# Performance work log

Measured on AMD Instinct MI355X. Metric: run time of the kernel, lower is better.

The kernel has to match this reference:

```python
import jax, jax.numpy as jnp
import numpy as np

N = 100000          # num nodes
K = 50              # num sampled neighbors per node (num_samples)
F_IN = 128          # in_features
F_OUT = 128         # out_features


def setup_inputs() -> dict:
    key = jax.random.key(0)
    k1, k2, k3, k4 = jax.random.split(key, 4)
    x = jax.random.normal(k1, (N, F_IN), dtype=jnp.float32)
    neighbors = jax.random.randint(k2, (N, K), 0, N, dtype=jnp.int64)
    stdv = 1.0 / np.sqrt(F_OUT)
    weight = jax.random.uniform(k3, (2 * F_IN, F_OUT), dtype=jnp.float32,
                                minval=-stdv, maxval=stdv)
    bias = jax.random.uniform(k4, (F_OUT,), dtype=jnp.float32,
                              minval=-stdv, maxval=stdv)
    return {"x": x, "neighbors": neighbors, "weight": weight, "bias": bias}


def reference(x, neighbors, weight, bias):
    # aggregate: gather sampled neighbor features and mean-reduce (aggregator='mean')
    # x[neighbors]: [N, K, F_IN] -> mean over K -> [N, F_IN]
    agg = jnp.mean(jnp.take(x, neighbors, axis=0), axis=1)
    # concat self + aggregated, linear, bias, relu
    h = jnp.concatenate([x, agg], axis=1)  # [N, 2*F_IN]
    out = h @ weight + bias                # [N, F_OUT]
    return jax.nn.relu(out)
```

## Files before the change

### kernel.cpp

```cpp
#include <hip/hip_runtime.h>
#include <hip/hip_bf16.h>
#include <stdint.h>

#define NN 100000
#define KN 50
#define FIN 128
#define FOUT 128
#define BM 64

typedef __attribute__((ext_vector_type(8))) short bf16x8;
typedef __attribute__((ext_vector_type(4))) float f32x4;
typedef __attribute__((ext_vector_type(2))) float f32x2;

__device__ __forceinline__ uint16_t f2b(float f){
  uint32_t x = __builtin_bit_cast(uint32_t, f);
  x += 0x7fffu + ((x >> 16) & 1u);
  return (uint16_t)(x >> 16);
}

__global__ void cast_fp8_kernel(const float* __restrict__ x, uint32_t* __restrict__ xf8){
  int i = blockIdx.x * blockDim.x + threadIdx.x;
  float4 v = *(const float4*)(x + (size_t)i * 4);
  uint32_t p = 0;
  p = __builtin_amdgcn_cvt_pk_fp8_f32(v.x, v.y, p, false);
  p = __builtin_amdgcn_cvt_pk_fp8_f32(v.z, v.w, p, true);
  xf8[i] = p;
}

__global__ void pack_w_kernel(const float* __restrict__ w, uint16_t* __restrict__ wp){
  int kt = blockIdx.x >> 3, nt = blockIdx.x & 7;
  int lane = threadIdx.x;
  int col = nt * 16 + (lane & 15);
  int k0  = kt * 32 + ((lane >> 4) << 3);
  uint16_t vals[8];
  #pragma unroll
  for (int i = 0; i < 8; i++) vals[i] = f2b(w[(k0 + i) * FOUT + col]);
  *(uint4*)(wp + ((size_t)(kt * 8 + nt) * 64 + lane) * 8) = *(const uint4*)vals;
}

__global__ void detect_kernel(const int* __restrict__ nb, int* __restrict__ flag){
  int i = blockIdx.x * blockDim.x + threadIdx.x;
  if (nb[2 * i + 1] != 0) *flag = 1;
}

#define CVT8(ACC, v)                                           \
  ACC[0] += __builtin_amdgcn_cvt_pk_f32_fp8((v).x, false);     \
  ACC[1] += __builtin_amdgcn_cvt_pk_f32_fp8((v).x, true);      \
  ACC[2] += __builtin_amdgcn_cvt_pk_f32_fp8((v).y, false);     \
  ACC[3] += __builtin_amdgcn_cvt_pk_f32_fp8((v).y, true);      \
  ACC[4] += __builtin_amdgcn_cvt_pk_f32_fp8((v).z, false);     \
  ACC[5] += __builtin_amdgcn_cvt_pk_f32_fp8((v).z, true);      \
  ACC[6] += __builtin_amdgcn_cvt_pk_f32_fp8((v).w, false);     \
  ACC[7] += __builtin_amdgcn_cvt_pk_f32_fp8((v).w, true);

__global__ __launch_bounds__(256, 4) void fused_kernel(
    const float* __restrict__ x,
    const uint8_t* __restrict__ xf8,
    const int* __restrict__ nbrs,
    const uint16_t* __restrict__ wp,
    const float* __restrict__ bias,
    const int* __restrict__ flag,
    float* __restrict__ out)
{
  __shared__ uint16_t h[BM][264];
  int* idxs = (int*)&h[0][0];
  const int tid  = threadIdx.x;
  const int wave = tid >> 6, lane = tid & 63;
  const int base = blockIdx.x * BM;
  const int sm = (*flag != 0) ? 1 : 2;

  {
    long long fb = (long long)(base + wave * 16) * KN;
    const long long fcap = (long long)NN * KN - 1;
    for (int t = lane; t < 16 * KN; t += 64){
      long long f = fb + t; if (f > fcap) f = fcap;
      idxs[wave * 16 * KN + t] = nbrs[f * sm];
    }
  }
  __syncthreads();

  const int g  = lane >> 3;
  const int fl = (lane & 7) * 16;
  const uint8_t* xfl = xf8 + fl;
  const int* ipA = idxs + wave * 16 * KN + g * KN;
  const int* ipB = ipA + 8 * KN;

  f32x2 accA[8], accB[8];
  #pragma unroll
  for (int i = 0; i < 8; i++){ accA[i] = (f32x2){0.f,0.f}; accB[i] = (f32x2){0.f,0.f}; }

  #pragma unroll 10
  for (int k = 0; k < KN; k++){
    int j = ipA[k];
    uint4 v = *(const uint4*)(xfl + ((size_t)(uint32_t)j << 7));
    CVT8(accA, v);
  }
  #pragma unroll 10
  for (int k = 0; k < KN; k++){
    int j = ipB[k];
    uint4 v = *(const uint4*)(xfl + ((size_t)(uint32_t)j << 7));
    CVT8(accB, v);
  }

  __syncthreads();

  {
    uint16_t oA[16], oB[16];
    #pragma unroll
    for (int i = 0; i < 8; i++){
      oA[2*i]   = f2b(accA[i].x * (1.0f / KN));
      oA[2*i+1] = f2b(accA[i].y * (1.0f / KN));
      oB[2*i]   = f2b(accB[i].x * (1.0f / KN));
      oB[2*i+1] = f2b(accB[i].y * (1.0f / KN));
    }
    uint16_t* dA = &h[wave * 16 + g][FIN + fl];
    uint16_t* dB = &h[wave * 16 + 8 + g][FIN + fl];
    *(uint4*)(dA)     = *(const uint4*)(oA);
    *(uint4*)(dA + 8) = *(const uint4*)(oA + 8);
    *(uint4*)(dB)     = *(const uint4*)(oB);
    *(uint4*)(dB + 8) = *(const uint4*)(oB + 8);
  }

  #pragma unroll
  for (int jj = 0; jj < 8; jj++){
    int ci = jj * 256 + tid;
    int r = ci >> 5, c = ci & 31;
    int node = base + r; if (node >= NN) node = NN - 1;
    float4 v = *(const float4*)(x + (size_t)node * FIN + c * 4);
    ushort4 o2; o2.x = f2b(v.x); o2.y = f2b(v.y); o2.z = f2b(v.z); o2.w = f2b(v.w);
    *(ushort4*)(&h[r][c * 4]) = o2;
  }

  bf16x8 bfr[8][2];
  #pragma unroll
  for (int kt = 0; kt < 8; kt++)
    #pragma unroll
    for (int ntl = 0; ntl < 2; ntl++){
      int nt = wave * 2 + ntl;
      bfr[kt][ntl] = *(const bf16x8*)(wp + ((size_t)(kt * 8 + nt) * 64 + lane) * 8);
    }

  __syncthreads();

  f32x4 acc[4][2];
  #pragma unroll
  for (int mt = 0; mt < 4; mt++)
    for (int n = 0; n < 2; n++) acc[mt][n] = (f32x4){0.f, 0.f, 0.f, 0.f};

  const int arow = lane & 15;
  const int ak   = (lane >> 4) << 3;
  #pragma unroll
  for (int kt = 0; kt < 8; kt++){
    #pragma unroll
    for (int mt = 0; mt < 4; mt++){
      bf16x8 af = *(const bf16x8*)(&h[mt * 16 + arow][kt * 32 + ak]);
      acc[mt][0] = __builtin_amdgcn_mfma_f32_16x16x32_bf16(af, bfr[kt][0], acc[mt][0], 0, 0, 0);
      acc[mt][1] = __builtin_amdgcn_mfma_f32_16x16x32_bf16(af, bfr[kt][1], acc[mt][1], 0, 0, 0);
    }
  }

  #pragma unroll
  for (int ntl = 0; ntl < 2; ntl++){
    int col = wave * 32 + ntl * 16 + (lane & 15);
    float bv = bias[col];
    #pragma unroll
    for (int mt = 0; mt < 4; mt++){
      #pragma unroll
      for (int i = 0; i < 4; i++){
        int row = mt * 16 + ((lane >> 4) << 2) + i;
        int node = base + row;
        if (node < NN){
          float v = acc[mt][ntl][i] + bv;
          out[(size_t)node * FOUT + col] = fmaxf(v, 0.f);
        }
      }
    }
  }
}

extern "C" void kernel_launch(void* const* d_in, const int* in_sizes, int n_in,
                              void* d_out, int out_size, void* d_ws, size_t ws_size,
                              hipStream_t stream){
  const float* x    = (const float*)d_in[0];
  const int*   nbrs = (const int*)d_in[1];
  const float* w    = (const float*)d_in[2];
  const float* bias = (const float*)d_in[3];
  float* out = (float*)d_out;

  uint8_t*  xf8  = (uint8_t*)d_ws;
  uint16_t* wp   = (uint16_t*)((char*)d_ws + (size_t)NN * FIN);
  int*      flag = (int*)((char*)d_ws + (size_t)NN * FIN + 65536);

  (void)hipMemsetAsync(flag, 0, 4, stream);
  cast_fp8_kernel<<<NN * FIN / 4 / 256, 256, 0, stream>>>(x, (uint32_t*)xf8);
  pack_w_kernel<<<64, 64, 0, stream>>>(w, wp);
  detect_kernel<<<32, 256, 0, stream>>>(nbrs, flag);
  fused_kernel<<<(NN + BM - 1) / BM, 256, 0, stream>>>(x, xf8, nbrs, wp, bias, flag, out);
}
```

Measured before the change: 123.1 us.

## Merge prep kernels into one launch and use 512-thread blocks in fused kernel

Combines the fp8 cast, weight packing and index-width detection kernels into a single prep launch partitioned by block index, removing two kernel launches. The fused kernel moves to 512 threads with eight waves, so each wave gathers 8 nodes instead of 16 and computes one 16-column MFMA tile instead of two. Weight fragments are now loaded per k-step inside the MMA loop instead of being preloaded, which cuts register use so more waves can be resident to hide gather latency. In exchange there are more waves per block sharing the barriers, and more redundant weight loads from global memory.

```diff
diff --git a/kernel.cpp b/kernel.cpp
--- a/kernel.cpp
+++ b/kernel.cpp
@@ -7,6 +7,9 @@
 #define FIN 128
 #define FOUT 128
 #define BM 64
+#define NCAST 12500
+#define NPACK 16
+#define NDET 32
 
 typedef __attribute__((ext_vector_type(8))) short bf16x8;
 typedef __attribute__((ext_vector_type(4))) float f32x4;
@@ -18,29 +21,33 @@
   return (uint16_t)(x >> 16);
 }
 
-__global__ void cast_fp8_kernel(const float* __restrict__ x, uint32_t* __restrict__ xf8){
-  int i = blockIdx.x * blockDim.x + threadIdx.x;
-  float4 v = *(const float4*)(x + (size_t)i * 4);
-  uint32_t p = 0;
-  p = __builtin_amdgcn_cvt_pk_fp8_f32(v.x, v.y, p, false);
-  p = __builtin_amdgcn_cvt_pk_fp8_f32(v.z, v.w, p, true);
-  xf8[i] = p;
-}
-
-__global__ void pack_w_kernel(const float* __restrict__ w, uint16_t* __restrict__ wp){
-  int kt = blockIdx.x >> 3, nt = blockIdx.x & 7;
-  int lane = threadIdx.x;
-  int col = nt * 16 + (lane & 15);
-  int k0  = kt * 32 + ((lane >> 4) << 3);
-  uint16_t vals[8];
-  #pragma unroll
-  for (int i = 0; i < 8; i++) vals[i] = f2b(w[(k0 + i) * FOUT + col]);
-  *(uint4*)(wp + ((size_t)(kt * 8 + nt) * 64 + lane) * 8) = *(const uint4*)vals;
-}
-
-__global__ void detect_kernel(const int* __restrict__ nb, int* __restrict__ flag){
-  int i = blockIdx.x * blockDim.x + threadIdx.x;
-  if (nb[2 * i + 1] != 0) *flag = 1;
+__global__ __launch_bounds__(256) void prep_kernel(
+    const float* __restrict__ x, uint32_t* __restrict__ xf8,
+    const float* __restrict__ w, uint16_t* __restrict__ wp,
+    const int* __restrict__ nb, int* __restrict__ flag)
+{
+  const int b = blockIdx.x, tid = threadIdx.x;
+  if (b < NCAST){
+    int i = b * 256 + tid;
+    float4 v = *(const float4*)(x + (size_t)i * 4);
+    uint32_t p = 0;
+    p = __builtin_amdgcn_cvt_pk_fp8_f32(v.x, v.y, p, false);
+    p = __builtin_amdgcn_cvt_pk_fp8_f32(v.z, v.w, p, true);
+    xf8[i] = p;
+  } else if (b < NCAST + NPACK){
+    int tp = (b - NCAST) * 256 + tid;
+    int bb = tp >> 6, lane = tp & 63;
+    int kt = bb >> 3, nt = bb & 7;
+    int col = nt * 16 + (lane & 15);
+    int k0  = kt * 32 + ((lane >> 4) << 3);
+    uint16_t vals[8];
+    #pragma unroll
+    for (int i = 0; i < 8; i++) vals[i] = f2b(w[(k0 + i) * FOUT + col]);
+    *(uint4*)(wp + ((size_t)(kt * 8 + nt) * 64 + lane) * 8) = *(const uint4*)vals;
+  } else {
+    int i = (b - NCAST - NPACK) * 256 + tid;
+    if (nb[2 * i + 1] != 0) *flag = 1;
+  }
 }
 
 #define CVT8(ACC, v)                                           \
@@ -53,7 +60,7 @@
   ACC[6] += __builtin_amdgcn_cvt_pk_f32_fp8((v).w, false);     \
   ACC[7] += __builtin_amdgcn_cvt_pk_f32_fp8((v).w, true);
 
-__global__ __launch_bounds__(256, 4) void fused_kernel(
+__global__ __launch_bounds__(512, 8) void fused_kernel(
     const float* __restrict__ x,
     const uint8_t* __restrict__ xf8,
     const int* __restrict__ nbrs,
@@ -70,11 +77,11 @@
   const int sm = (*flag != 0) ? 1 : 2;
 
   {
-    long long fb = (long long)(base + wave * 16) * KN;
+    long long fb = (long long)(base + wave * 8) * KN;
     const long long fcap = (long long)NN * KN - 1;
-    for (int t = lane; t < 16 * KN; t += 64){
+    for (int t = lane; t < 8 * KN; t += 64){
       long long f = fb + t; if (f > fcap) f = fcap;
-      idxs[wave * 16 * KN + t] = nbrs[f * sm];
+      idxs[wave * 8 * KN + t] = nbrs[f * sm];
     }
   }
   __syncthreads();
@@ -82,48 +89,36 @@
   const int g  = lane >> 3;
   const int fl = (lane & 7) * 16;
   const uint8_t* xfl = xf8 + fl;
-  const int* ipA = idxs + wave * 16 * KN + g * KN;
-  const int* ipB = ipA + 8 * KN;
+  const int* ip = idxs + wave * 8 * KN + g * KN;
 
-  f32x2 accA[8], accB[8];
+  f32x2 acc8[8];
   #pragma unroll
-  for (int i = 0; i < 8; i++){ accA[i] = (f32x2){0.f,0.f}; accB[i] = (f32x2){0.f,0.f}; }
+  for (int i = 0; i < 8; i++) acc8[i] = (f32x2){0.f, 0.f};
 
   #pragma unroll 10
   for (int k = 0; k < KN; k++){
-    int j = ipA[k];
+    int j = ip[k];
     uint4 v = *(const uint4*)(xfl + ((size_t)(uint32_t)j << 7));
-    CVT8(accA, v);
-  }
-  #pragma unroll 10
-  for (int k = 0; k < KN; k++){
-    int j = ipB[k];
-    uint4 v = *(const uint4*)(xfl + ((size_t)(uint32_t)j << 7));
-    CVT8(accB, v);
+    CVT8(acc8, v);
   }
 
   __syncthreads();
 
   {
-    uint16_t oA[16], oB[16];
+    uint16_t o[16];
     #pragma unroll
     for (int i = 0; i < 8; i++){
-      oA[2*i]   = f2b(accA[i].x * (1.0f / KN));
-      oA[2*i+1] = f2b(accA[i].y * (1.0f / KN));
-      oB[2*i]   = f2b(accB[i].x * (1.0f / KN));
-      oB[2*i+1] = f2b(accB[i].y * (1.0f / KN));
+      o[2*i]   = f2b(acc8[i].x * (1.0f / KN));
+      o[2*i+1] = f2b(acc8[i].y * (1.0f / KN));
     }
-    uint16_t* dA = &h[wave * 16 + g][FIN + fl];
-    uint16_t* dB = &h[wave * 16 + 8 + g][FIN + fl];
-    *(uint4*)(dA)     = *(const uint4*)(oA);
-    *(uint4*)(dA + 8) = *(const uint4*)(oA + 8);
-    *(uint4*)(dB)     = *(const uint4*)(oB);
-    *(uint4*)(dB + 8) = *(const uint4*)(oB + 8);
+    uint16_t* d = &h[wave * 8 + g][FIN + fl];
+    *(uint4*)(d)     = *(const uint4*)(o);
+    *(uint4*)(d + 8) = *(const uint4*)(o + 8);
   }
 
   #pragma unroll
-  for (int jj = 0; jj < 8; jj++){
-    int ci = jj * 256 + tid;
+  for (int jj = 0; jj < 4; jj++){
+    int ci = jj * 512 + tid;
     int r = ci >> 5, c = ci & 31;
     int node = base + r; if (node >= NN) node = NN - 1;
     float4 v = *(const float4*)(x + (size_t)node * FIN + c * 4);
@@ -131,37 +126,26 @@
     *(ushort4*)(&h[r][c * 4]) = o2;
   }
 
-  bf16x8 bfr[8][2];
-  #pragma unroll
-  for (int kt = 0; kt < 8; kt++)
-    #pragma unroll
-    for (int ntl = 0; ntl < 2; ntl++){
-      int nt = wave * 2 + ntl;
-      bfr[kt][ntl] = *(const bf16x8*)(wp + ((size_t)(kt * 8 + nt) * 64 + lane) * 8);
-    }
-
   __syncthreads();
 
-  f32x4 acc[4][2];
+  f32x4 acc[4];
   #pragma unroll
-  for (int mt = 0; mt < 4; mt++)
-    for (int n = 0; n < 2; n++) acc[mt][n] = (f32x4){0.f, 0.f, 0.f, 0.f};
+  for (int mt = 0; mt < 4; mt++) acc[mt] = (f32x4){0.f, 0.f, 0.f, 0.f};
 
   const int arow = lane & 15;
   const int ak   = (lane >> 4) << 3;
   #pragma unroll
   for (int kt = 0; kt < 8; kt++){
+    bf16x8 bfrk = *(const bf16x8*)(wp + ((size_t)(kt * 8 + wave) * 64 + lane) * 8);
     #pragma unroll
     for (int mt = 0; mt < 4; mt++){
       bf16x8 af = *(const bf16x8*)(&h[mt * 16 + arow][kt * 32 + ak]);
-      acc[mt][0] = __builtin_amdgcn_mfma_f32_16x16x32_bf16(af, bfr[kt][0], acc[mt][0], 0, 0, 0);
-      acc[mt][1] = __builtin_amdgcn_mfma_f32_16x16x32_bf16(af, bfr[kt][1], acc[mt][1], 0, 0, 0);
+      acc[mt] = __builtin_amdgcn_mfma_f32_16x16x32_bf16(af, bfrk, acc[mt], 0, 0, 0);
     }
   }
 
-  #pragma unroll
-  for (int ntl = 0; ntl < 2; ntl++){
-    int col = wave * 32 + ntl * 16 + (lane & 15);
+  {
+    int col = wave * 16 + (lane & 15);
     float bv = bias[col];
     #pragma unroll
     for (int mt = 0; mt < 4; mt++){
@@ -170,7 +154,7 @@
         int row = mt * 16 + ((lane >> 4) << 2) + i;
         int node = base + row;
         if (node < NN){
-          float v = acc[mt][ntl][i] + bv;
+          float v = acc[mt][i] + bv;
           out[(size_t)node * FOUT + col] = fmaxf(v, 0.f);
         }
       }
@@ -192,8 +176,8 @@
   int*      flag = (int*)((char*)d_ws + (size_t)NN * FIN + 65536);
 
   (void)hipMemsetAsync(flag, 0, 4, stream);
-  cast_fp8_kernel<<<NN * FIN / 4 / 256, 256, 0, stream>>>(x, (uint32_t*)xf8);
-  pack_w_kernel<<<64, 64, 0, stream>>>(w, wp);
-  detect_kernel<<<32, 256, 0, stream>>>(nbrs, flag);
-  fused_kernel<<<(NN + BM - 1) / BM, 256, 0, stream>>>(x, xf8, nbrs, wp, bias, flag, out);
+  prep_kernel<<<NCAST + NPACK + NDET, 256, 0, stream>>>(
+      x, (uint32_t*)xf8, w, wp, (const int*)nbrs, flag);
+  fused_kernel<<<(NN + BM - 1) / BM, 512, 0, stream>>>(
+      x, xf8, nbrs, wp, bias, flag, out);
 }
```

Result: faster. 104.7 us (median of 2 runs) (-15.0%).
